# Kernel optimization log

Measured on AMD Instinct MI355X. Metric: run time of the kernel, lower is better.

Reference implementation:

```python
import jax, jax.numpy as jnp
import numpy as np

N_IN = 1024
N_OUT = 1024
L, B = 2048, 16


def setup_inputs() -> dict:
    key = jax.random.key(0)
    k1, k2 = jax.random.split(key, 2)
    val = (3.0 / N_IN) ** 0.5  # matches init_weight uniform range
    return {
        "x": jax.random.normal(k1, (L, B, N_IN), dtype=jnp.float32),
        "c0": jnp.zeros((B, N_OUT), dtype=jnp.float32),
        "weight": jax.random.uniform(k2, (N_IN, 3 * N_OUT), dtype=jnp.float32, minval=-val, maxval=val),
        "bias": jnp.zeros((2 * N_OUT,), dtype=jnp.float32),
    }


def reference(x, c0, weight, bias):
    # x: (L, B, n_in); weight: (n_in, 3*n_out); bias: (2*n_out,)
    Lx, Bx, _ = x.shape
    # u_ = x @ W, viewed as (L, B, n_out, k=3); bidir=1 dropped
    u = (x.reshape(Lx * Bx, N_IN) @ weight).reshape(Lx, Bx, N_OUT, 3)
    x_tilde = u[..., 0]                                  # (L, B, d)
    forget = jax.nn.sigmoid(u[..., 1] + bias[:N_OUT])    # (L, B, d)
    # sequential SRU recurrence: c_t = (c_{t-1} - x~_t) * f_t + x~_t
    def step(c_prev, inputs):
        xt, ft = inputs
        c = (c_prev - xt) * ft + xt
        return c, c
    c_final, cs = jax.lax.scan(step, c0, (x_tilde, forget))
    h = jnp.tanh(cs)  # activation_type == 1 (tanh); no highway, no dropout (eval)
    return h, c_final
```

## Files before the change

kernel.cpp:

```cpp
#include <hip/hip_runtime.h>


typedef __attribute__((ext_vector_type(8))) short short8;
typedef __attribute__((ext_vector_type(4))) float f32x4;

#define L_SEQ 2048
#define BATCH 16
#define NIN   1024
#define NOUT  1024
#define MROWS (L_SEQ * BATCH)
#define NCOLS (2 * NOUT)
#define ROWELEMS (BATCH * NOUT)
#define NCHUNK 32
#define CHLEN  64
#define NT 16

__device__ __forceinline__ unsigned short f2bf(float f) {
  unsigned u = __float_as_uint(f);
  u += 0x7fffu + ((u >> 16) & 1u);
  return (unsigned short)(u >> 16);
}
__device__ __forceinline__ float bf2f(unsigned short b) {
  return __uint_as_float(((unsigned)b) << 16);
}
__device__ __forceinline__ float sigmoidf_(float x) {
  return __builtin_amdgcn_rcpf(1.f + __expf(-x));
}
__device__ __forceinline__ float fast_tanh(float x) {
  float ax = fabsf(x);
  float t = __expf(-2.f * ax);
  float r = (1.f - t) * __builtin_amdgcn_rcpf(1.f + t);
  return copysignf(r, x);
}

#define GLL16(gptr, lptr)                                              \
  __builtin_amdgcn_global_load_lds(                                    \
      (const __attribute__((address_space(1))) void*)(gptr),           \
      (__attribute__((address_space(3))) void*)(lptr), 16, 0, 0)

__global__ __launch_bounds__(256) void cvt_x_k(const float* __restrict__ x,
                                               unsigned short* __restrict__ o) {
  size_t i = ((size_t)blockIdx.x * 256 + threadIdx.x) * 8;
  const float4* p = (const float4*)(x + i);
  float4 a = p[0], b = p[1];
  union { unsigned short s[8]; uint4 v; } r;
  r.s[0] = f2bf(a.x); r.s[1] = f2bf(a.y); r.s[2] = f2bf(a.z); r.s[3] = f2bf(a.w);
  r.s[4] = f2bf(b.x); r.s[5] = f2bf(b.y); r.s[6] = f2bf(b.z); r.s[7] = f2bf(b.w);
  *(uint4*)(o + i) = r.v;
}

__global__ __launch_bounds__(256) void pack_w_k(const float* __restrict__ W,
                                                unsigned short* __restrict__ Bp) {
  __shared__ float tile[64][97];
  int n0 = blockIdx.x * 64;
  int k0 = blockIdx.y * 64;
  int c0 = 3 * (n0 >> 1);
  int tid = threadIdx.x;
  for (int idx = tid; idx < 64 * 96; idx += 256) {
    int r = idx / 96, c = idx - r * 96;
    tile[r][c] = W[(size_t)(k0 + r) * (3 * NOUT) + c0 + c];
  }
  __syncthreads();
#pragma unroll
  for (int q = 0; q < 2; ++q) {
    int pos = tid * 2 + q;
    int dn = pos >> 3;
    int j8 = (pos & 7) * 8;
    int cl = 3 * (dn >> 1) + (dn & 1);
    union { unsigned short s[8]; uint4 v; } r;
#pragma unroll
    for (int j = 0; j < 8; ++j) r.s[j] = f2bf(tile[j8 + j][cl]);
    *(uint4*)(Bp + (size_t)(n0 + dn) * NIN + k0 + j8) = r.v;
  }
}

#define BARR __builtin_amdgcn_s_barrier()
#define SCHED0 __builtin_amdgcn_sched_barrier(0)
#define VMCNT(n) asm volatile("s_waitcnt vmcnt(" #n ")" ::: "memory")

#define STAGE_A(bufc, ha, kt)                                                   \
  do {                                                                          \
    GLL16(pga##ha##0 + (kt) * 64, lds + (bufc) * 32768 + (ha) * 16384 + tid * 16);      \
    GLL16(pga##ha##1 + (kt) * 64, lds + (bufc) * 32768 + (ha) * 16384 + 8192 + tid * 16); \
  } while (0)
#define STAGE_B(bufc, hb, kt)                                                   \
  do {                                                                          \
    GLL16(pgb##hb##0 + (kt) * 64, lds + 65536 + (bufc) * 32768 + (hb) * 16384 + tid * 16); \
    GLL16(pgb##hb##1 + (kt) * 64, lds + 65536 + (bufc) * 32768 + (hb) * 16384 + 8192 + tid * 16); \
  } while (0)

#define LDA(DST, bufc, half)                                                    \
  _Pragma("unroll") for (int i = 0; i < 4; ++i) {                               \
    DST[i][0] = *(const short8*)(lds + (bufc) * 32768 + (half) * 16384 +        \
                                 (rowAb + i * 16) * 128 + colX0);               \
    DST[i][1] = *(const short8*)(lds + (bufc) * 32768 + (half) * 16384 +        \
                                 (rowAb + i * 16) * 128 + colX1);               \
  }
#define LDB(DST, bufc, half)                                                    \
  _Pragma("unroll") for (int j = 0; j < 2; ++j) {                               \
    DST[j][0] = *(const short8*)(lds + 65536 + (bufc) * 32768 + (half) * 16384 + \
                                 (rowBb + j * 16) * 128 + colX0);               \
    DST[j][1] = *(const short8*)(lds + 65536 + (bufc) * 32768 + (half) * 16384 + \
                                 (rowBb + j * 16) * 128 + colX1);               \
  }

#define MM(Q, AF, BF)                                                           \
  _Pragma("unroll") for (int i = 0; i < 4; ++i)                                 \
  _Pragma("unroll") for (int j = 0; j < 2; ++j) {                               \
    Q[i][j] = __builtin_amdgcn_mfma_f32_16x16x32_bf16(AF[i][0], BF[j][0], Q[i][j], 0, 0, 0); \
    Q[i][j] = __builtin_amdgcn_mfma_f32_16x16x32_bf16(AF[i][1], BF[j][1], Q[i][j], 0, 0, 0); \
  }

#define PH2_TAIL(Q1, BF1, Q2, BF2)                                              \
  BARR;                                                                         \
  __builtin_amdgcn_s_setprio(1);                                                \
  MM(Q1, af, BF1);                                                              \
  MM(Q2, af, BF2);                                                              \
  __builtin_amdgcn_s_setprio(0);                                                \
  BARR;                                                                         \
  SCHED0

#define PH2_TAILV(Q1, BF1, Q2, BF2)                                             \
  BARR;                                                                         \
  __builtin_amdgcn_s_setprio(1);                                                \
  MM(Q1, af, BF1);                                                              \
  MM(Q2, af, BF2);                                                              \
  __builtin_amdgcn_s_setprio(0);                                                \
  VMCNT(4);                                                                     \
  BARR;                                                                         \
  SCHED0

#define PH2_TAILV0(Q1, BF1, Q2, BF2)                                            \
  BARR;                                                                         \
  __builtin_amdgcn_s_setprio(1);                                                \
  MM(Q1, af, BF1);                                                              \
  MM(Q2, af, BF2);                                                              \
  __builtin_amdgcn_s_setprio(0);                                                \
  VMCNT(0);                                                                     \
  BARR;                                                                         \
  SCHED0

#define EPI(Q, qm, qn)                                                          \
  do {                                                                          \
    _Pragma("unroll") for (int i = 0; i < 4; ++i)                               \
    _Pragma("unroll") for (int j = 0; j < 2; ++j) {                             \
      int n = n0 + (qn) * 128 + wn * 32 + j * 16 + nc;                          \
      float bsel = bias[n >> 1];                                                \
      _Pragma("unroll") for (int r = 0; r < 4; ++r) {                           \
        int m = m0 + (qm) * 128 + wm * 64 + i * 16 + mr + r;                    \
        float v = Q[i][j][r];                                                   \
        if (isf) v = sigmoidf_(v + bsel);                                       \
        U[(size_t)m * NCOLS + n] = f2bf(v);                                     \
      }                                                                         \
    }                                                                           \
  } while (0)

__global__ __launch_bounds__(512, 2) void gemm8_k(const unsigned short* __restrict__ A,
                                                  const unsigned short* __restrict__ B,
                                                  const float* __restrict__ bias,
                                                  unsigned short* __restrict__ U) {
  __shared__ __align__(16) char lds[131072];
  const int K = NIN;
  int tid = threadIdx.x;
  int wave = tid >> 6;
  int lane = tid & 63;
  int wm = wave >> 2;
  int wn = wave & 3;
  int lr = lane & 15;
  int hi = lane >> 4;

  int bi = blockIdx.x;
  int t = (bi & 7) * 128 + (bi >> 3);
  int n0 = (t & 7) << 8;
  int m0 = (t >> 3) << 8;

  int rowAb = wm * 64 + lr;
  int rowBb = wn * 32 + lr;
  int swz = (lr & 7) << 4;
  int colX0 = (hi * 16) ^ swz;
  int colX1 = (64 + hi * 16) ^ swz;

  int row0 = tid >> 3;
  int gch = (tid & 7) ^ (row0 & 7);
  const unsigned short* pga00 = A + (size_t)(m0 + row0) * K + gch * 8;
  const unsigned short* pga01 = pga00 + (size_t)64 * K;
  const unsigned short* pga10 = pga00 + (size_t)128 * K;
  const unsigned short* pga11 = pga00 + (size_t)192 * K;
  const unsigned short* pgb00 = B + (size_t)(n0 + row0) * K + gch * 8;
  const unsigned short* pgb01 = pgb00 + (size_t)64 * K;
  const unsigned short* pgb10 = pgb00 + (size_t)128 * K;
  const unsigned short* pgb11 = pgb00 + (size_t)192 * K;

  f32x4 zero = {0.f, 0.f, 0.f, 0.f};
  f32x4 acc00[4][2], acc01[4][2], acc11[4][2], acc10[4][2];
#pragma unroll
  for (int i = 0; i < 4; ++i)
#pragma unroll
    for (int j = 0; j < 2; ++j) {
      acc00[i][j] = zero; acc01[i][j] = zero;
      acc11[i][j] = zero; acc10[i][j] = zero;
    }

  short8 af[4][2], bq0[2][2], bq1[2][2];

  STAGE_A(0, 0, 0); STAGE_A(0, 1, 0); STAGE_B(0, 0, 0); STAGE_B(0, 1, 0);
  STAGE_A(1, 0, 1); STAGE_B(1, 1, 1);
  VMCNT(4);
  BARR;
  SCHED0;

  for (int it = 0; it < NT / 2 - 1; ++it) {
    int kt = it * 2;
    int k1 = kt + 1, k2 = kt + 2, k3 = kt + 3;
    STAGE_B(1, 0, k1); STAGE_A(1, 1, k1);
    LDA(af, 0, 0); LDB(bq0, 0, 0); LDB(bq1, 0, 1);
    PH2_TAIL(acc00, bq0, acc01, bq1);
    STAGE_A(0, 0, k2); STAGE_B(0, 1, k2);
    LDA(af, 0, 1);
    PH2_TAILV(acc11, bq1, acc10, bq0);
    STAGE_A(0, 1, k2); STAGE_B(0, 0, k2);
    LDA(af, 1, 0); LDB(bq0, 1, 0); LDB(bq1, 1, 1);
    PH2_TAIL(acc00, bq0, acc01, bq1);
    STAGE_A(1, 0, k3); STAGE_B(1, 1, k3);
    LDA(af, 1, 1);
    PH2_TAILV(acc11, bq1, acc10, bq0);
  }

  {
    STAGE_B(1, 0, 15); STAGE_A(1, 1, 15);
    LDA(af, 0, 0); LDB(bq0, 0, 0); LDB(bq1, 0, 1);
    PH2_TAIL(acc00, bq0, acc01, bq1);
    LDA(af, 0, 1);
    PH2_TAILV0(acc11, bq1, acc10, bq0);
    LDA(af, 1, 0); LDB(bq0, 1, 0); LDB(bq1, 1, 1);
    PH2_TAIL(acc00, bq0, acc01, bq1);
    LDA(af, 1, 1);
    PH2_TAIL(acc11, bq1, acc10, bq0);
  }

  int mr = hi * 4;
  int nc = lane & 15;
  bool isf = nc & 1;
  EPI(acc00, 0, 0);
  EPI(acc01, 0, 1);
  EPI(acc11, 1, 1);
  EPI(acc10, 1, 0);
}

__global__ __launch_bounds__(256) void scan_p1(const unsigned int* __restrict__ U2,
                                               float2* __restrict__ AV) {
  int tid = threadIdx.x;
  int bid = blockIdx.x;
  int bd = ((bid >> 7) << 10) + ((bid & 3) << 8) + tid;
  int chunk = (bid >> 2) & 31;
  const unsigned int* up = U2 + (size_t)chunk * CHLEN * ROWELEMS + bd;
  float a = 1.f, v = 0.f;
  for (int t0 = 0; t0 < CHLEN; t0 += 8) {
    unsigned int w[8];
#pragma unroll
    for (int j = 0; j < 8; ++j) w[j] = up[(size_t)(t0 + j) * ROWELEMS];
#pragma unroll
    for (int j = 0; j < 8; ++j) {
      float xt = bf2f((unsigned short)(w[j] & 0xffffu));
      float f  = bf2f((unsigned short)(w[j] >> 16));
      v = f * v + (1.f - f) * xt;
      a = a * f;
    }
  }
  AV[(size_t)chunk * ROWELEMS + bd] = make_float2(a, v);
}

__global__ __launch_bounds__(256) void scan_p2(const float2* __restrict__ AV,
                                               const float* __restrict__ c0,
                                               float* __restrict__ CS,
                                               float* __restrict__ out) {
  int bd = blockIdx.x * 256 + threadIdx.x;
  float c = c0[bd];
  float2 av[NCHUNK];
#pragma unroll
  for (int k = 0; k < NCHUNK; ++k) av[k] = AV[(size_t)k * ROWELEMS + bd];
#pragma unroll
  for (int k = 0; k < NCHUNK; ++k) {
    CS[(size_t)k * ROWELEMS + bd] = c;
    c = av[k].x * c + av[k].y;
  }
  out[(size_t)MROWS * NOUT + bd] = c;
}

__global__ __launch_bounds__(256) void scan_p3(const unsigned int* __restrict__ U2,
                                               const float* __restrict__ CS,
                                               float* __restrict__ out) {
  int tid = threadIdx.x;
  int bid = blockIdx.x;
  int bd = ((bid >> 7) << 10) + ((bid & 3) << 8) + tid;
  int chunk = (bid >> 2) & 31;
  float c = CS[(size_t)chunk * ROWELEMS + bd];
  const unsigned int* up = U2 + (size_t)chunk * CHLEN * ROWELEMS + bd;
  float* op = out + (size_t)chunk * CHLEN * ROWELEMS + bd;
  for (int t0 = 0; t0 < CHLEN; t0 += 8) {
    unsigned int w[8];
#pragma unroll
    for (int j = 0; j < 8; ++j) w[j] = up[(size_t)(t0 + j) * ROWELEMS];
#pragma unroll
    for (int j = 0; j < 8; ++j) {
      float xt = bf2f((unsigned short)(w[j] & 0xffffu));
      float f  = bf2f((unsigned short)(w[j] >> 16));
      c = (c - xt) * f + xt;
      op[(size_t)(t0 + j) * ROWELEMS] = fast_tanh(c);
    }
  }
}

extern "C" void kernel_launch(void* const* d_in, const int* in_sizes, int n_in,
                              void* d_out, int out_size, void* d_ws, size_t ws_size,
                              hipStream_t stream) {
  const float* x    = (const float*)d_in[0];
  const float* c0   = (const float*)d_in[1];
  const float* W    = (const float*)d_in[2];
  const float* bias = (const float*)d_in[3];
  float* out = (float*)d_out;

  char* ws = (char*)d_ws;
  unsigned short* Abf = (unsigned short*)ws;
  unsigned short* Bp  = (unsigned short*)(ws + ((size_t)64 << 20));
  unsigned short* U   = (unsigned short*)(ws + ((size_t)68 << 20));
  float2* AV = (float2*)ws;
  float*  CS = (float*)(ws + ((size_t)4 << 20));

  cvt_x_k<<<MROWS * NIN / (256 * 8), 256, 0, stream>>>(x, Abf);
  pack_w_k<<<dim3(NCOLS / 64, NIN / 64), 256, 0, stream>>>(W, Bp);
  gemm8_k<<<1024, 512, 0, stream>>>(Abf, Bp, bias, U);
  scan_p1<<<2048, 256, 0, stream>>>((const unsigned int*)U, AV);
  scan_p2<<<64, 256, 0, stream>>>(AV, c0, CS, out);
  scan_p3<<<2048, 256, 0, stream>>>((const unsigned int*)U, CS, out);
}
```

Measured before the change: 251.2 us.

## Make GEMM persistent over four M tiles with prefetch across tile boundaries

The GEMM grid shrinks from 1024 to 256 workgroups, and each one loops over four consecutive 256-row M tiles that share the same B column tile. The prefetch of the next M tile's first K slices is issued during the last K iteration of the current tile, so the pipeline does not drain and refill between tiles. The goal is to amortize launch and prologue cost and hide the pipeline fill behind compute. In exchange, the epilogue stores now sit inside the main loop, and the 256 workgroups may underfill the GPU's compute units, since launch bounds allow 2 per CU.

```diff
diff --git a/kernel.cpp b/kernel.cpp
--- a/kernel.cpp
+++ b/kernel.cpp
@@ -80,13 +80,13 @@
 
 #define STAGE_A(bufc, ha, kt)                                                   \
   do {                                                                          \
-    GLL16(pga##ha##0 + (kt) * 64, lds + (bufc) * 32768 + (ha) * 16384 + tid * 16);      \
-    GLL16(pga##ha##1 + (kt) * 64, lds + (bufc) * 32768 + (ha) * 16384 + 8192 + tid * 16); \
+    GLL16(pa##ha##0 + (kt) * 64, lds + (bufc) * 32768 + (ha) * 16384 + tid * 16);      \
+    GLL16(pa##ha##1 + (kt) * 64, lds + (bufc) * 32768 + (ha) * 16384 + 8192 + tid * 16); \
   } while (0)
 #define STAGE_B(bufc, hb, kt)                                                   \
   do {                                                                          \
-    GLL16(pgb##hb##0 + (kt) * 64, lds + 65536 + (bufc) * 32768 + (hb) * 16384 + tid * 16); \
-    GLL16(pgb##hb##1 + (kt) * 64, lds + 65536 + (bufc) * 32768 + (hb) * 16384 + 8192 + tid * 16); \
+    GLL16(pb##hb##0 + (kt) * 64, lds + 65536 + (bufc) * 32768 + (hb) * 16384 + tid * 16); \
+    GLL16(pb##hb##1 + (kt) * 64, lds + 65536 + (bufc) * 32768 + (hb) * 16384 + 8192 + tid * 16); \
   } while (0)
 
 #define LDA(DST, bufc, half)                                                    \
@@ -140,20 +140,43 @@
   BARR;                                                                         \
   SCHED0
 
-#define EPI(Q, qm, qn)                                                          \
+#define EPI(Q, qm, qn, M0)                                                      \
   do {                                                                          \
     _Pragma("unroll") for (int i = 0; i < 4; ++i)                               \
     _Pragma("unroll") for (int j = 0; j < 2; ++j) {                             \
       int n = n0 + (qn) * 128 + wn * 32 + j * 16 + nc;                          \
       float bsel = bias[n >> 1];                                                \
       _Pragma("unroll") for (int r = 0; r < 4; ++r) {                           \
-        int m = m0 + (qm) * 128 + wm * 64 + i * 16 + mr + r;                    \
+        int m = (M0) + (qm) * 128 + wm * 64 + i * 16 + mr + r;                  \
         float v = Q[i][j][r];                                                   \
         if (isf) v = sigmoidf_(v + bsel);                                       \
         U[(size_t)m * NCOLS + n] = f2bf(v);                                     \
       }                                                                         \
     }                                                                           \
   } while (0)
+
+#define ZACC                                                                    \
+  do {                                                                          \
+    _Pragma("unroll") for (int i = 0; i < 4; ++i)                               \
+    _Pragma("unroll") for (int j = 0; j < 2; ++j) {                             \
+      acc00[i][j] = zero; acc01[i][j] = zero;                                   \
+      acc11[i][j] = zero; acc10[i][j] = zero;                                   \
+    }                                                                           \
+  } while (0)
+
+#define ITER_BODY(k1, k2, k3)                                                   \
+  STAGE_B(1, 0, k1); STAGE_A(1, 1, k1);                                         \
+  LDA(af, 0, 0); LDB(bq0, 0, 0); LDB(bq1, 0, 1);                                \
+  PH2_TAIL(acc00, bq0, acc01, bq1);                                             \
+  STAGE_A(0, 0, k2); STAGE_B(0, 1, k2);                                         \
+  LDA(af, 0, 1);                                                                \
+  PH2_TAILV(acc11, bq1, acc10, bq0);                                            \
+  STAGE_A(0, 1, k2); STAGE_B(0, 0, k2);                                         \
+  LDA(af, 1, 0); LDB(bq0, 1, 0); LDB(bq1, 1, 1);                                \
+  PH2_TAIL(acc00, bq0, acc01, bq1);                                             \
+  STAGE_A(1, 0, k3); STAGE_B(1, 1, k3);                                         \
+  LDA(af, 1, 1);                                                                \
+  PH2_TAILV(acc11, bq1, acc10, bq0);
 
 __global__ __launch_bounds__(512, 2) void gemm8_k(const unsigned short* __restrict__ A,
                                                   const unsigned short* __restrict__ B,
@@ -170,9 +193,9 @@
   int hi = lane >> 4;
 
   int bi = blockIdx.x;
-  int t = (bi & 7) * 128 + (bi >> 3);
+  int t = (bi & 7) * 32 + (bi >> 3);
   int n0 = (t & 7) << 8;
-  int m0 = (t >> 3) << 8;
+  int m_base = (t >> 3) << 10;
 
   int rowAb = wm * 64 + lr;
   int rowBb = wn * 32 + lr;
@@ -182,24 +205,18 @@
 
   int row0 = tid >> 3;
   int gch = (tid & 7) ^ (row0 & 7);
-  const unsigned short* pga00 = A + (size_t)(m0 + row0) * K + gch * 8;
-  const unsigned short* pga01 = pga00 + (size_t)64 * K;
-  const unsigned short* pga10 = pga00 + (size_t)128 * K;
-  const unsigned short* pga11 = pga00 + (size_t)192 * K;
-  const unsigned short* pgb00 = B + (size_t)(n0 + row0) * K + gch * 8;
-  const unsigned short* pgb01 = pgb00 + (size_t)64 * K;
-  const unsigned short* pgb10 = pgb00 + (size_t)128 * K;
-  const unsigned short* pgb11 = pgb00 + (size_t)192 * K;
+  const unsigned short* pa00 = A + (size_t)(m_base + row0) * K + gch * 8;
+  const unsigned short* pa01 = pa00 + (size_t)64 * K;
+  const unsigned short* pa10 = pa00 + (size_t)128 * K;
+  const unsigned short* pa11 = pa00 + (size_t)192 * K;
+  const unsigned short* pb00 = B + (size_t)(n0 + row0) * K + gch * 8;
+  const unsigned short* pb01 = pb00 + (size_t)64 * K;
+  const unsigned short* pb10 = pb00 + (size_t)128 * K;
+  const unsigned short* pb11 = pb00 + (size_t)192 * K;
 
   f32x4 zero = {0.f, 0.f, 0.f, 0.f};
   f32x4 acc00[4][2], acc01[4][2], acc11[4][2], acc10[4][2];
-#pragma unroll
-  for (int i = 0; i < 4; ++i)
-#pragma unroll
-    for (int j = 0; j < 2; ++j) {
-      acc00[i][j] = zero; acc01[i][j] = zero;
-      acc11[i][j] = zero; acc10[i][j] = zero;
-    }
+  ZACC;
 
   short8 af[4][2], bq0[2][2], bq1[2][2];
 
@@ -209,42 +226,54 @@
   BARR;
   SCHED0;
 
-  for (int it = 0; it < NT / 2 - 1; ++it) {
-    int kt = it * 2;
-    int k1 = kt + 1, k2 = kt + 2, k3 = kt + 3;
-    STAGE_B(1, 0, k1); STAGE_A(1, 1, k1);
-    LDA(af, 0, 0); LDB(bq0, 0, 0); LDB(bq1, 0, 1);
-    PH2_TAIL(acc00, bq0, acc01, bq1);
-    STAGE_A(0, 0, k2); STAGE_B(0, 1, k2);
-    LDA(af, 0, 1);
-    PH2_TAILV(acc11, bq1, acc10, bq0);
-    STAGE_A(0, 1, k2); STAGE_B(0, 0, k2);
-    LDA(af, 1, 0); LDB(bq0, 1, 0); LDB(bq1, 1, 1);
-    PH2_TAIL(acc00, bq0, acc01, bq1);
-    STAGE_A(1, 0, k3); STAGE_B(1, 1, k3);
-    LDA(af, 1, 1);
-    PH2_TAILV(acc11, bq1, acc10, bq0);
-  }
-
-  {
-    STAGE_B(1, 0, 15); STAGE_A(1, 1, 15);
-    LDA(af, 0, 0); LDB(bq0, 0, 0); LDB(bq1, 0, 1);
-    PH2_TAIL(acc00, bq0, acc01, bq1);
-    LDA(af, 0, 1);
-    PH2_TAILV0(acc11, bq1, acc10, bq0);
-    LDA(af, 1, 0); LDB(bq0, 1, 0); LDB(bq1, 1, 1);
-    PH2_TAIL(acc00, bq0, acc01, bq1);
-    LDA(af, 1, 1);
-    PH2_TAIL(acc11, bq1, acc10, bq0);
-  }
-
   int mr = hi * 4;
   int nc = lane & 15;
   bool isf = nc & 1;
-  EPI(acc00, 0, 0);
-  EPI(acc01, 0, 1);
-  EPI(acc11, 1, 1);
-  EPI(acc10, 1, 0);
+  int m0v = m_base;
+
+  for (int mi = 0; mi < 4; ++mi) {
+    for (int it = 0; it < NT / 2 - 1; ++it) {
+      int kt = it * 2;
+      int k1 = kt + 1, k2 = kt + 2, k3 = kt + 3;
+      ITER_BODY(k1, k2, k3)
+    }
+    if (mi < 3) {
+      STAGE_B(1, 0, 15); STAGE_A(1, 1, 15);
+      LDA(af, 0, 0); LDB(bq0, 0, 0); LDB(bq1, 0, 1);
+      PH2_TAIL(acc00, bq0, acc01, bq1);
+      pa00 += (size_t)256 * K; pa01 += (size_t)256 * K;
+      pa10 += (size_t)256 * K; pa11 += (size_t)256 * K;
+      STAGE_A(0, 0, 0); STAGE_B(0, 1, 0);
+      LDA(af, 0, 1);
+      PH2_TAILV(acc11, bq1, acc10, bq0);
+      STAGE_A(0, 1, 0); STAGE_B(0, 0, 0);
+      LDA(af, 1, 0); LDB(bq0, 1, 0); LDB(bq1, 1, 1);
+      PH2_TAIL(acc00, bq0, acc01, bq1);
+      STAGE_A(1, 0, 1); STAGE_B(1, 1, 1);
+      LDA(af, 1, 1);
+      PH2_TAILV(acc11, bq1, acc10, bq0);
+      EPI(acc00, 0, 0, m0v);
+      EPI(acc01, 0, 1, m0v);
+      EPI(acc11, 1, 1, m0v);
+      EPI(acc10, 1, 0, m0v);
+      ZACC;
+      m0v += 256;
+    } else {
+      STAGE_B(1, 0, 15); STAGE_A(1, 1, 15);
+      LDA(af, 0, 0); LDB(bq0, 0, 0); LDB(bq1, 0, 1);
+      PH2_TAIL(acc00, bq0, acc01, bq1);
+      LDA(af, 0, 1);
+      PH2_TAILV0(acc11, bq1, acc10, bq0);
+      LDA(af, 1, 0); LDB(bq0, 1, 0); LDB(bq1, 1, 1);
+      PH2_TAIL(acc00, bq0, acc01, bq1);
+      LDA(af, 1, 1);
+      PH2_TAIL(acc11, bq1, acc10, bq0);
+      EPI(acc00, 0, 0, m0v);
+      EPI(acc01, 0, 1, m0v);
+      EPI(acc11, 1, 1, m0v);
+      EPI(acc10, 1, 0, m0v);
+    }
+  }
 }
 
 __global__ __launch_bounds__(256) void scan_p1(const unsigned int* __restrict__ U2,
@@ -329,7 +358,7 @@
 
   cvt_x_k<<<MROWS * NIN / (256 * 8), 256, 0, stream>>>(x, Abf);
   pack_w_k<<<dim3(NCOLS / 64, NIN / 64), 256, 0, stream>>>(W, Bp);
-  gemm8_k<<<1024, 512, 0, stream>>>(Abf, Bp, bias, U);
+  gemm8_k<<<256, 512, 0, stream>>>(Abf, Bp, bias, U);
   scan_p1<<<2048, 256, 0, stream>>>((const unsigned int*)U, AV);
   scan_p2<<<64, 256, 0, stream>>>(AV, c0, CS, out);
   scan_p3<<<2048, 256, 0, stream>>>((const unsigned int*)U, CS, out);
```

Result: slower. 528.8 us (+110.5%).
